# Performance work log

Measured on AMD Instinct MI355X. Metric: run time of the kernel, lower is better.

The kernel has to match this reference:

```python
import jax, jax.numpy as jnp
import numpy as np

EMBED = 1024
HIDDEN = 64  # embed_size // n_heads
B, L = 8, 4096


def setup_inputs() -> dict:
    key = jax.random.key(0)
    k1, k2, k3, k4, k5, k6, k7 = jax.random.split(key, 7)
    query = jax.random.normal(k1, (B, L, EMBED), dtype=jnp.float32)
    key_t = jax.random.normal(k2, (B, L, EMBED), dtype=jnp.float32)
    value = jax.random.normal(k3, (B, L, EMBED), dtype=jnp.float32)
    mask = jax.random.randint(k4, (B, L, L), 0, 2).astype(jnp.bool_)
    # nn.Linear(embed, hidden, bias=False) weights have shape (hidden, embed)
    s = 1.0 / np.sqrt(EMBED)
    WQ = jax.random.uniform(k5, (HIDDEN, EMBED), jnp.float32, -s, s)
    WK = jax.random.uniform(k6, (HIDDEN, EMBED), jnp.float32, -s, s)
    WV = jax.random.uniform(k7, (HIDDEN, EMBED), jnp.float32, -s, s)
    return {"query": query, "key": key_t, "value": value, "mask": mask,
            "WQ": WQ, "WK": WK, "WV": WV}


def reference(query, key, value, mask, WQ, WK, WV):
    # Projections: y = x @ W.T  (Linear without bias)
    Q = jnp.einsum('ble,he->blh', query, WQ)   # [B,L,H]
    K = jnp.einsum('ble,he->blh', key, WK)
    V = jnp.einsum('ble,he->blh', value, WV)
    scale = 1.0 / jnp.sqrt(jnp.asarray(Q.shape[-1], Q.dtype))
    scores = jnp.einsum('bqh,bkh->bqk', Q, K) * scale   # [B,L,L]
    scores = jnp.where(mask, -jnp.inf, scores)
    attn = jax.nn.softmax(scores, axis=-1)
    # dropout p=0.0 -> identity
    return jnp.einsum('bqk,bkh->bqh', attn, V)           # [B,L,H]
```

## Files before the change

### kernel.cpp

```cpp
#include <hip/hip_runtime.h>
#include <hip/hip_bf16.h>

#define NB 8
#define LL 4096
#define EE 1024
#define HH 64

typedef unsigned short u16;
typedef unsigned char u8;
typedef unsigned int u32;
typedef unsigned long long u64;
using bf16x8 = __attribute__((ext_vector_type(8))) short;
using f32x4  = __attribute__((ext_vector_type(4))) float;

__device__ __forceinline__ short f2bf(float f) {
    __hip_bfloat16 h = __float2bfloat16(f);
    return __builtin_bit_cast(short, h);
}

__device__ __forceinline__ bf16x8 pack8(const float4 a, const float4 b) {
    bf16x8 r;
    r[0] = f2bf(a.x); r[1] = f2bf(a.y); r[2] = f2bf(a.z); r[3] = f2bf(a.w);
    r[4] = f2bf(b.x); r[5] = f2bf(b.y); r[6] = f2bf(b.z); r[7] = f2bf(b.w);
    return r;
}

__global__ __launch_bounds__(256) void proj_kernel(
    const float* __restrict__ Xq, const float* __restrict__ Xk, const float* __restrict__ Xv,
    const float* __restrict__ Wq, const float* __restrict__ Wk, const float* __restrict__ Wv,
    u16* __restrict__ Oq, u16* __restrict__ Ok, u16* __restrict__ Ovt)
{
    __shared__ u16 Xs[2][64][72];
    __shared__ u16 Ws2[2][64][72];

    const int which = blockIdx.y;
    const float* X = (which == 0) ? Xq : (which == 1) ? Xk : Xv;
    const float* W = (which == 0) ? Wq : (which == 1) ? Wk : Wv;
    const float scale = (which == 0) ? 0.125f : 1.0f;

    const int tid  = threadIdx.x;
    const int lane = tid & 63;
    const int w    = tid >> 6;
    const int g    = lane >> 4;
    const int c    = lane & 15;
    const int m0   = blockIdx.x * 64;
    const int r    = tid >> 2;
    const int cb   = (tid & 3) * 16;

    const float* xrow = X + (size_t)(m0 + r) * EE + cb;
    const float* wrow = W + (size_t)r * EE + cb;

    float4 xr[4], wr[4];
    #pragma unroll
    for (int i = 0; i < 4; ++i) {
        xr[i] = reinterpret_cast<const float4*>(xrow)[i];
        wr[i] = reinterpret_cast<const float4*>(wrow)[i];
    }
    *reinterpret_cast<bf16x8*>(&Xs[0][r][cb])      = pack8(xr[0], xr[1]);
    *reinterpret_cast<bf16x8*>(&Xs[0][r][cb + 8])  = pack8(xr[2], xr[3]);
    *reinterpret_cast<bf16x8*>(&Ws2[0][r][cb])     = pack8(wr[0], wr[1]);
    *reinterpret_cast<bf16x8*>(&Ws2[0][r][cb + 8]) = pack8(wr[2], wr[3]);
    __syncthreads();

    f32x4 acc[4];
    #pragma unroll
    for (int t = 0; t < 4; ++t) acc[t] = (f32x4){0.f, 0.f, 0.f, 0.f};

    for (int s = 0; s < 16; ++s) {
        const int curb = s & 1, nxtb = curb ^ 1;
        if (s < 15) {
            #pragma unroll
            for (int i = 0; i < 4; ++i) {
                xr[i] = reinterpret_cast<const float4*>(xrow + (s + 1) * 64)[i];
                wr[i] = reinterpret_cast<const float4*>(wrow + (s + 1) * 64)[i];
            }
        }
        __builtin_amdgcn_s_setprio(1);
        #pragma unroll
        for (int kk = 0; kk < 2; ++kk) {
            bf16x8 a = *reinterpret_cast<const bf16x8*>(&Xs[curb][16*w + c][kk*32 + 8*g]);
            #pragma unroll
            for (int t = 0; t < 4; ++t) {
                bf16x8 bb = *reinterpret_cast<const bf16x8*>(&Ws2[curb][16*t + c][kk*32 + 8*g]);
                acc[t] = __builtin_amdgcn_mfma_f32_16x16x32_bf16(a, bb, acc[t], 0, 0, 0);
            }
        }
        __builtin_amdgcn_s_setprio(0);
        if (s < 15) {
            *reinterpret_cast<bf16x8*>(&Xs[nxtb][r][cb])      = pack8(xr[0], xr[1]);
            *reinterpret_cast<bf16x8*>(&Xs[nxtb][r][cb + 8])  = pack8(xr[2], xr[3]);
            *reinterpret_cast<bf16x8*>(&Ws2[nxtb][r][cb])     = pack8(wr[0], wr[1]);
            *reinterpret_cast<bf16x8*>(&Ws2[nxtb][r][cb + 8]) = pack8(wr[2], wr[3]);
        }
        __syncthreads();
    }

    if (which < 2) {
        u16* O = (which == 0) ? Oq : Ok;
        #pragma unroll
        for (int t = 0; t < 4; ++t)
            #pragma unroll
            for (int q = 0; q < 4; ++q) {
                const int mrow = m0 + 16*w + 4*g + q;
                O[(size_t)mrow * HH + 16*t + c] = (u16)f2bf(acc[t][q] * scale);
            }
    } else {
        const int bidx = m0 >> 12;
        #pragma unroll
        for (int t = 0; t < 4; ++t)
            #pragma unroll
            for (int q = 0; q < 4; ++q) {
                const int l = (m0 & (LL - 1)) + 16*w + 4*g + q;
                Ovt[((size_t)bidx * HH + 16*t + c) * LL + l] = (u16)f2bf(acc[t][q]);
            }
    }
}

__global__ __launch_bounds__(256) void attn_kernel(
    const u16* __restrict__ Qb, const u16* __restrict__ Kb, const u16* __restrict__ Vt,
    const int* __restrict__ mask, float* __restrict__ out)
{
    __shared__ u16 Ks[2][64][72];
    __shared__ u16 Vts[2][64][72];
    __shared__ u16 Ps[4][16][72];
    __shared__ u64 Pnl[2][4][64];

    const int b    = blockIdx.y;
    const int q0   = blockIdx.x * 64;
    const int tid  = threadIdx.x;
    const int lane = tid & 63;
    const int w    = tid >> 6;
    const int g    = lane >> 4;
    const int c    = lane & 15;
    const int r    = tid >> 2;
    const int cb   = (tid & 3) * 16;
    const int mrr  = tid >> 4;
    const int mcc  = tid & 15;

    const u16* kbase = Kb + (size_t)b * LL * HH;
    const u16* vbase = Vt + (size_t)b * HH * LL;
    const int* mbase0 = mask + (size_t)b * LL * LL + (size_t)(q0 + mrr) * LL + mcc * 16;

    bf16x8 qf[2];
    {
        const u16* qp = Qb + ((size_t)b * LL + q0 + 16*w + c) * HH;
        qf[0] = *reinterpret_cast<const bf16x8*>(qp + 8*g);
        qf[1] = *reinterpret_cast<const bf16x8*>(qp + 32 + 8*g);
    }

    bf16x8 kra, krb, vra, vrb;
    int4 mi0, mi1, mi2, mi3;

    #define LOADKV(kt_) do {                                                   \
        kra = *reinterpret_cast<const bf16x8*>(kbase + (size_t)((kt_)*64 + r) * HH + cb);       \
        krb = *reinterpret_cast<const bf16x8*>(kbase + (size_t)((kt_)*64 + r) * HH + cb + 8);   \
        vra = *reinterpret_cast<const bf16x8*>(vbase + (size_t)r * LL + (kt_)*64 + cb);         \
        vrb = *reinterpret_cast<const bf16x8*>(vbase + (size_t)r * LL + (kt_)*64 + cb + 8);     \
    } while (0)
    #define WRITEKV(buf_) do {                                                 \
        *reinterpret_cast<bf16x8*>(&Ks[buf_][r][cb])      = kra;               \
        *reinterpret_cast<bf16x8*>(&Ks[buf_][r][cb + 8])  = krb;               \
        *reinterpret_cast<bf16x8*>(&Vts[buf_][r][cb])     = vra;               \
        *reinterpret_cast<bf16x8*>(&Vts[buf_][r][cb + 8]) = vrb;               \
    } while (0)
    #define MLOAD(w_, p_) do {                                                 \
        const int4* _mp = reinterpret_cast<const int4*>(mbase0 + (size_t)(16*(p_)) * LL + (w_)*256); \
        mi0 = _mp[0]; mi1 = _mp[1]; mi2 = _mp[2]; mi3 = _mp[3];                \
    } while (0)
    #define MPACK(pb_, p_) do {                                                \
        u32 _bb =  (u32)(mi0.x != 0)        | ((u32)(mi0.y != 0) << 1)         \
                | ((u32)(mi0.z != 0) << 2)  | ((u32)(mi0.w != 0) << 3)         \
                | ((u32)(mi1.x != 0) << 4)  | ((u32)(mi1.y != 0) << 5)         \
                | ((u32)(mi1.z != 0) << 6)  | ((u32)(mi1.w != 0) << 7)         \
                | ((u32)(mi2.x != 0) << 8)  | ((u32)(mi2.y != 0) << 9)         \
                | ((u32)(mi2.z != 0) << 10) | ((u32)(mi2.w != 0) << 11)        \
                | ((u32)(mi3.x != 0) << 12) | ((u32)(mi3.y != 0) << 13)        \
                | ((u32)(mi3.z != 0) << 14) | ((u32)(mi3.w != 0) << 15);       \
        ((u16*)&Pnl[pb_][mcc >> 2][16*(p_) + mrr])[mcc & 3] = (u16)_bb;        \
    } while (0)

    f32x4 acc[4];
    float lpart[4];
    #pragma unroll
    for (int t = 0; t < 4; ++t) acc[t] = (f32x4){0.f, 0.f, 0.f, 0.f};
    #pragma unroll
    for (int q = 0; q < 4; ++q) lpart[q] = 0.f;

    #define TILE_BODY(CUR, PB, TI) do {                                        \
        f32x4 s[4];                                                            \
        __builtin_amdgcn_s_setprio(1);                                         \
        _Pragma("unroll")                                                      \
        for (int t = 0; t < 4; ++t) {                                          \
            s[t] = (f32x4){0.f, 0.f, 0.f, 0.f};                                \
            _Pragma("unroll")                                                  \
            for (int kk = 0; kk < 2; ++kk) {                                   \
                bf16x8 bfr = *reinterpret_cast<const bf16x8*>(&Ks[CUR][16*t + c][kk*32 + 8*g]); \
                s[t] = __builtin_amdgcn_mfma_f32_16x16x32_bf16(qf[kk], bfr, s[t], 0, 0, 0);     \
            }                                                                  \
        }                                                                      \
        __builtin_amdgcn_s_setprio(0);                                         \
        u64 mw0 = Pnl[PB][TI][16*w + 4*g + 0];                                 \
        u64 mw1 = Pnl[PB][TI][16*w + 4*g + 1];                                 \
        u64 mw2 = Pnl[PB][TI][16*w + 4*g + 2];                                 \
        u64 mw3 = Pnl[PB][TI][16*w + 4*g + 3];                                 \
        u32 mlo[4], mhi[4];                                                    \
        mlo[0] = (u32)mw0; mhi[0] = (u32)(mw0 >> 32);                          \
        mlo[1] = (u32)mw1; mhi[1] = (u32)(mw1 >> 32);                          \
        mlo[2] = (u32)mw2; mhi[2] = (u32)(mw2 >> 32);                          \
        mlo[3] = (u32)mw3; mhi[3] = (u32)(mw3 >> 32);                          \
        _Pragma("unroll")                                                      \
        for (int t = 0; t < 4; ++t)                                            \
            _Pragma("unroll")                                                  \
            for (int q = 0; q < 4; ++q) {                                      \
                u32 wsel = (t < 2) ? mlo[q] : mhi[q];                          \
                u32 bit = (wsel >> ((t & 1) * 16 + c)) & 1u;                   \
                float p = bit ? 0.f : __expf(s[t][q]);                         \
                lpart[q] += p;                                                 \
                Ps[w][4*g + q][16*t + c] = (u16)f2bf(p);                       \
            }                                                                  \
        __builtin_amdgcn_s_setprio(1);                                         \
        _Pragma("unroll")                                                      \
        for (int kk = 0; kk < 2; ++kk) {                                       \
            bf16x8 pa = *reinterpret_cast<const bf16x8*>(&Ps[w][c][kk*32 + 8*g]);               \
            _Pragma("unroll")                                                  \
            for (int t = 0; t < 4; ++t) {                                      \
                bf16x8 vfr = *reinterpret_cast<const bf16x8*>(&Vts[CUR][16*t + c][kk*32 + 8*g]);\
                acc[t] = __builtin_amdgcn_mfma_f32_16x16x32_bf16(pa, vfr, acc[t], 0, 0, 0);     \
            }                                                                  \
        }                                                                      \
        __builtin_amdgcn_s_setprio(0);                                         \
    } while (0)

    LOADKV(0);
    MLOAD(0, 0); MPACK(0, 0);
    MLOAD(0, 1); MPACK(0, 1);
    MLOAD(0, 2); MPACK(0, 2);
    MLOAD(0, 3); MPACK(0, 3);
    WRITEKV(0);
    __syncthreads();

    for (int win = 0; win < 16; ++win) {
        const int base = 4 * win;
        const int pcur = win & 1, pnxt = pcur ^ 1;
        const bool more = (win + 1 < 16);

        LOADKV(base + 1);
        if (more) MLOAD(win + 1, 0);
        TILE_BODY(0, pcur, 0);
        WRITEKV(1);
        if (more) MPACK(pnxt, 0);
        __syncthreads();

        LOADKV(base + 2);
        if (more) MLOAD(win + 1, 1);
        TILE_BODY(1, pcur, 1);
        WRITEKV(0);
        if (more) MPACK(pnxt, 1);
        __syncthreads();

        LOADKV(base + 3);
        if (more) MLOAD(win + 1, 2);
        TILE_BODY(0, pcur, 2);
        WRITEKV(1);
        if (more) MPACK(pnxt, 2);
        __syncthreads();

        if (more) { LOADKV(base + 4); MLOAD(win + 1, 3); }
        TILE_BODY(1, pcur, 3);
        if (more) { WRITEKV(0); MPACK(pnxt, 3); }
        __syncthreads();
    }

    #pragma unroll
    for (int off = 8; off >= 1; off >>= 1)
        #pragma unroll
        for (int q = 0; q < 4; ++q)
            lpart[q] += __shfl_xor(lpart[q], off, 64);
    #pragma unroll
    for (int q = 0; q < 4; ++q) {
        const float inv = 1.0f / lpart[q];
        const size_t row = (size_t)b * LL + q0 + 16*w + 4*g + q;
        #pragma unroll
        for (int t = 0; t < 4; ++t)
            out[row * HH + 16*t + c] = acc[t][q] * inv;
    }
}

extern "C" void kernel_launch(void* const* d_in, const int* in_sizes, int n_in,
                              void* d_out, int out_size, void* d_ws, size_t ws_size,
                              hipStream_t stream) {
    const float* query = (const float*)d_in[0];
    const float* key_t = (const float*)d_in[1];
    const float* value = (const float*)d_in[2];
    const int*   mask  = (const int*)d_in[3];
    const float* WQ    = (const float*)d_in[4];
    const float* WK    = (const float*)d_in[5];
    const float* WV    = (const float*)d_in[6];
    float* out = (float*)d_out;

    const size_t nqkv = (size_t)NB * LL * HH;
    u16* Qb  = (u16*)d_ws;
    u16* Kb  = Qb + nqkv;
    u16* Vtb = Kb + nqkv;

    dim3 pgrid(NB * LL / 64, 3);
    proj_kernel<<<pgrid, 256, 0, stream>>>(query, key_t, value, WQ, WK, WV, Qb, Kb, Vtb);

    dim3 agrid(LL / 64, NB);
    attn_kernel<<<agrid, 256, 0, stream>>>(Qb, Kb, Vtb, mask, out);
}
```

Measured before the change: 218.4 us.

## Process two KV tiles per barrier with swizzled unpadded LDS and per-phase mask packing

Restructures the attention main loop so each iteration prefetches and computes two 64-key tiles at a time, with four K/V LDS buffers instead of two. This halves the number of __syncthreads. LDS K/V tiles drop their padding and use an XOR swizzle to avoid bank conflicts. Mask loading changes so each thread packs 32 mask bits for its own row per phase. The cost is more registers for the doubled prefetch, which may reduce occupancy.

```diff
diff --git a/kernel.cpp b/kernel.cpp
--- a/kernel.cpp
+++ b/kernel.cpp
@@ -120,10 +120,10 @@
     const u16* __restrict__ Qb, const u16* __restrict__ Kb, const u16* __restrict__ Vt,
     const int* __restrict__ mask, float* __restrict__ out)
 {
-    __shared__ u16 Ks[2][64][72];
-    __shared__ u16 Vts[2][64][72];
+    __shared__ u16 Ks[4][64][64];
+    __shared__ u16 Vts[4][64][64];
     __shared__ u16 Ps[4][16][72];
-    __shared__ u64 Pnl[2][4][64];
+    __shared__ u64 Pnl[2][2][64];
 
     const int b    = blockIdx.y;
     const int q0   = blockIdx.x * 64;
@@ -133,13 +133,14 @@
     const int g    = lane >> 4;
     const int c    = lane & 15;
     const int r    = tid >> 2;
-    const int cb   = (tid & 3) * 16;
-    const int mrr  = tid >> 4;
-    const int mcc  = tid & 15;
+    const int ch   = tid & 3;
+    const int cb   = ch * 16;
+    const int swzw = (r & 7) << 3;
+    const int swzr = (c & 7) << 3;
 
     const u16* kbase = Kb + (size_t)b * LL * HH;
     const u16* vbase = Vt + (size_t)b * HH * LL;
-    const int* mbase0 = mask + (size_t)b * LL * LL + (size_t)(q0 + mrr) * LL + mcc * 16;
+    const int* mbase = mask + (size_t)b * LL * LL + (size_t)(q0 + r) * LL + ch * 32;
 
     bf16x8 qf[2];
     {
@@ -148,35 +149,46 @@
         qf[1] = *reinterpret_cast<const bf16x8*>(qp + 32 + 8*g);
     }
 
-    bf16x8 kra, krb, vra, vrb;
-    int4 mi0, mi1, mi2, mi3;
-
-    #define LOADKV(kt_) do {                                                   \
-        kra = *reinterpret_cast<const bf16x8*>(kbase + (size_t)((kt_)*64 + r) * HH + cb);       \
-        krb = *reinterpret_cast<const bf16x8*>(kbase + (size_t)((kt_)*64 + r) * HH + cb + 8);   \
-        vra = *reinterpret_cast<const bf16x8*>(vbase + (size_t)r * LL + (kt_)*64 + cb);         \
-        vrb = *reinterpret_cast<const bf16x8*>(vbase + (size_t)r * LL + (kt_)*64 + cb + 8);     \
-    } while (0)
-    #define WRITEKV(buf_) do {                                                 \
-        *reinterpret_cast<bf16x8*>(&Ks[buf_][r][cb])      = kra;               \
-        *reinterpret_cast<bf16x8*>(&Ks[buf_][r][cb + 8])  = krb;               \
-        *reinterpret_cast<bf16x8*>(&Vts[buf_][r][cb])     = vra;               \
-        *reinterpret_cast<bf16x8*>(&Vts[buf_][r][cb + 8]) = vrb;               \
-    } while (0)
-    #define MLOAD(w_, p_) do {                                                 \
-        const int4* _mp = reinterpret_cast<const int4*>(mbase0 + (size_t)(16*(p_)) * LL + (w_)*256); \
+    bf16x8 k0a, k0b, v0a, v0b, k1a, k1b, v1a, v1b;
+    int4 mi0, mi1, mi2, mi3, mi4, mi5, mi6, mi7;
+
+    #define LOADKV0(kt_) do {                                                  \
+        k0a = *reinterpret_cast<const bf16x8*>(kbase + (size_t)((kt_)*64 + r) * HH + cb);       \
+        k0b = *reinterpret_cast<const bf16x8*>(kbase + (size_t)((kt_)*64 + r) * HH + cb + 8);   \
+        v0a = *reinterpret_cast<const bf16x8*>(vbase + (size_t)r * LL + (kt_)*64 + cb);         \
+        v0b = *reinterpret_cast<const bf16x8*>(vbase + (size_t)r * LL + (kt_)*64 + cb + 8);     \
+    } while (0)
+    #define LOADKV1(kt_) do {                                                  \
+        k1a = *reinterpret_cast<const bf16x8*>(kbase + (size_t)((kt_)*64 + r) * HH + cb);       \
+        k1b = *reinterpret_cast<const bf16x8*>(kbase + (size_t)((kt_)*64 + r) * HH + cb + 8);   \
+        v1a = *reinterpret_cast<const bf16x8*>(vbase + (size_t)r * LL + (kt_)*64 + cb);         \
+        v1b = *reinterpret_cast<const bf16x8*>(vbase + (size_t)r * LL + (kt_)*64 + cb + 8);     \
+    } while (0)
+    #define WRITEKV0(buf_) do {                                                \
+        *reinterpret_cast<bf16x8*>(&Ks[buf_][r][cb ^ swzw])        = k0a;      \
+        *reinterpret_cast<bf16x8*>(&Ks[buf_][r][(cb ^ swzw) ^ 8])  = k0b;      \
+        *reinterpret_cast<bf16x8*>(&Vts[buf_][r][cb ^ swzw])       = v0a;      \
+        *reinterpret_cast<bf16x8*>(&Vts[buf_][r][(cb ^ swzw) ^ 8]) = v0b;      \
+    } while (0)
+    #define WRITEKV1(buf_) do {                                                \
+        *reinterpret_cast<bf16x8*>(&Ks[buf_][r][cb ^ swzw])        = k1a;      \
+        *reinterpret_cast<bf16x8*>(&Ks[buf_][r][(cb ^ swzw) ^ 8])  = k1b;      \
+        *reinterpret_cast<bf16x8*>(&Vts[buf_][r][cb ^ swzw])       = v1a;      \
+        *reinterpret_cast<bf16x8*>(&Vts[buf_][r][(cb ^ swzw) ^ 8]) = v1b;      \
+    } while (0)
+    #define MLOADPH(T_) do {                                                   \
+        const int4* _mp = reinterpret_cast<const int4*>(mbase + (T_) * 64);    \
         mi0 = _mp[0]; mi1 = _mp[1]; mi2 = _mp[2]; mi3 = _mp[3];                \
-    } while (0)
-    #define MPACK(pb_, p_) do {                                                \
-        u32 _bb =  (u32)(mi0.x != 0)        | ((u32)(mi0.y != 0) << 1)         \
-                | ((u32)(mi0.z != 0) << 2)  | ((u32)(mi0.w != 0) << 3)         \
-                | ((u32)(mi1.x != 0) << 4)  | ((u32)(mi1.y != 0) << 5)         \
-                | ((u32)(mi1.z != 0) << 6)  | ((u32)(mi1.w != 0) << 7)         \
-                | ((u32)(mi2.x != 0) << 8)  | ((u32)(mi2.y != 0) << 9)         \
-                | ((u32)(mi2.z != 0) << 10) | ((u32)(mi2.w != 0) << 11)        \
-                | ((u32)(mi3.x != 0) << 12) | ((u32)(mi3.y != 0) << 13)        \
-                | ((u32)(mi3.z != 0) << 14) | ((u32)(mi3.w != 0) << 15);       \
-        ((u16*)&Pnl[pb_][mcc >> 2][16*(p_) + mrr])[mcc & 3] = (u16)_bb;        \
+        mi4 = _mp[4]; mi5 = _mp[5]; mi6 = _mp[6]; mi7 = _mp[7];                \
+    } while (0)
+    #define PB32(v_, sh_) ( ((u32)((v_).x != 0) << (sh_))                      \
+                          | ((u32)((v_).y != 0) << ((sh_)+1))                  \
+                          | ((u32)((v_).z != 0) << ((sh_)+2))                  \
+                          | ((u32)((v_).w != 0) << ((sh_)+3)) )
+    #define MPACKPH(pb_) do {                                                  \
+        u32 _bits = PB32(mi0,0) | PB32(mi1,4)  | PB32(mi2,8)  | PB32(mi3,12)   \
+                  | PB32(mi4,16) | PB32(mi5,20) | PB32(mi6,24) | PB32(mi7,28); \
+        ((u32*)&Pnl[pb_][ch >> 1][r])[ch & 1] = _bits;                         \
     } while (0)
 
     f32x4 acc[4];
@@ -186,7 +198,7 @@
     #pragma unroll
     for (int q = 0; q < 4; ++q) lpart[q] = 0.f;
 
-    #define TILE_BODY(CUR, PB, TI) do {                                        \
+    #define TILE_BODY(BUF, PB, TI) do {                                        \
         f32x4 s[4];                                                            \
         __builtin_amdgcn_s_setprio(1);                                         \
         _Pragma("unroll")                                                      \
@@ -194,7 +206,8 @@
             s[t] = (f32x4){0.f, 0.f, 0.f, 0.f};                                \
             _Pragma("unroll")                                                  \
             for (int kk = 0; kk < 2; ++kk) {                                   \
-                bf16x8 bfr = *reinterpret_cast<const bf16x8*>(&Ks[CUR][16*t + c][kk*32 + 8*g]); \
+                bf16x8 bfr = *reinterpret_cast<const bf16x8*>(                 \
+                    &Ks[BUF][16*t + c][((kk<<5) | (g<<3)) ^ swzr]);            \
                 s[t] = __builtin_amdgcn_mfma_f32_16x16x32_bf16(qf[kk], bfr, s[t], 0, 0, 0);     \
             }                                                                  \
         }                                                                      \
@@ -221,53 +234,42 @@
         __builtin_amdgcn_s_setprio(1);                                         \
         _Pragma("unroll")                                                      \
         for (int kk = 0; kk < 2; ++kk) {                                       \
-            bf16x8 pa = *reinterpret_cast<const bf16x8*>(&Ps[w][c][kk*32 + 8*g]);               \
+            bf16x8 pfr = *reinterpret_cast<const bf16x8*>(&Ps[w][c][kk*32 + 8*g]);              \
             _Pragma("unroll")                                                  \
             for (int t = 0; t < 4; ++t) {                                      \
-                bf16x8 vfr = *reinterpret_cast<const bf16x8*>(&Vts[CUR][16*t + c][kk*32 + 8*g]);\
-                acc[t] = __builtin_amdgcn_mfma_f32_16x16x32_bf16(pa, vfr, acc[t], 0, 0, 0);     \
+                bf16x8 vfr = *reinterpret_cast<const bf16x8*>(                 \
+                    &Vts[BUF][16*t + c][((kk<<5) | (g<<3)) ^ swzr]);           \
+                acc[t] = __builtin_amdgcn_mfma_f32_16x16x32_bf16(pfr, vfr, acc[t], 0, 0, 0);    \
             }                                                                  \
         }                                                                      \
         __builtin_amdgcn_s_setprio(0);                                         \
     } while (0)
 
-    LOADKV(0);
-    MLOAD(0, 0); MPACK(0, 0);
-    MLOAD(0, 1); MPACK(0, 1);
-    MLOAD(0, 2); MPACK(0, 2);
-    MLOAD(0, 3); MPACK(0, 3);
-    WRITEKV(0);
+    LOADKV0(0);
+    LOADKV1(1);
+    MLOADPH(0);
+    WRITEKV0(0);
+    WRITEKV1(1);
+    MPACKPH(0);
     __syncthreads();
 
-    for (int win = 0; win < 16; ++win) {
-        const int base = 4 * win;
-        const int pcur = win & 1, pnxt = pcur ^ 1;
-        const bool more = (win + 1 < 16);
-
-        LOADKV(base + 1);
-        if (more) MLOAD(win + 1, 0);
-        TILE_BODY(0, pcur, 0);
-        WRITEKV(1);
-        if (more) MPACK(pnxt, 0);
-        __syncthreads();
-
-        LOADKV(base + 2);
-        if (more) MLOAD(win + 1, 1);
-        TILE_BODY(1, pcur, 1);
-        WRITEKV(0);
-        if (more) MPACK(pnxt, 1);
-        __syncthreads();
-
-        LOADKV(base + 3);
-        if (more) MLOAD(win + 1, 2);
-        TILE_BODY(0, pcur, 2);
-        WRITEKV(1);
-        if (more) MPACK(pnxt, 2);
-        __syncthreads();
-
-        if (more) { LOADKV(base + 4); MLOAD(win + 1, 3); }
-        TILE_BODY(1, pcur, 3);
-        if (more) { WRITEKV(0); MPACK(pnxt, 3); }
+    for (int f = 0; f < 32; ++f) {
+        const int pa = f & 1;
+        const int ba = (f & 1) * 2;
+        const int bn = ba ^ 2;
+
+        if (f < 31) {
+            LOADKV0(2*f + 2);
+            LOADKV1(2*f + 3);
+            MLOADPH(2*f + 2);
+        }
+        TILE_BODY(ba,     pa, 0);
+        TILE_BODY(ba + 1, pa, 1);
+        if (f < 31) {
+            WRITEKV0(bn);
+            WRITEKV1(bn + 1);
+            MPACKPH(pa ^ 1);
+        }
         __syncthreads();
     }
 
```

Result: slower. 263.7 us (+20.7%).

## Deepen mask prefetch to two stages and interleave batches in grid order

Applied to the files above, without the earlier changes.

The mask load for a tile group is now issued two tile-steps ahead using two alternating register sets (A/B), instead of one step ahead, so the global-memory latency of the large int32 mask stream has more compute to hide behind. The grid is flattened to 1D with batch index in the low bits, so neighbouring blocks work on different batches. This changes which blocks share K/V in L2 at a given time. The deeper prefetch costs an extra 16 registers per thread for the second mask buffer, which may lower occupancy.

```diff
diff --git a/kernel.cpp b/kernel.cpp
--- a/kernel.cpp
+++ b/kernel.cpp
@@ -125,8 +125,8 @@
     __shared__ u16 Ps[4][16][72];
     __shared__ u64 Pnl[2][4][64];
 
-    const int b    = blockIdx.y;
-    const int q0   = blockIdx.x * 64;
+    const int b    = blockIdx.x & 7;
+    const int q0   = (blockIdx.x >> 3) * 64;
     const int tid  = threadIdx.x;
     const int lane = tid & 63;
     const int w    = tid >> 6;
@@ -149,7 +149,7 @@
     }
 
     bf16x8 kra, krb, vra, vrb;
-    int4 mi0, mi1, mi2, mi3;
+    int4 mA0, mA1, mA2, mA3, mB0, mB1, mB2, mB3;
 
     #define LOADKV(kt_) do {                                                   \
         kra = *reinterpret_cast<const bf16x8*>(kbase + (size_t)((kt_)*64 + r) * HH + cb);       \
@@ -163,20 +163,21 @@
         *reinterpret_cast<bf16x8*>(&Vts[buf_][r][cb])     = vra;               \
         *reinterpret_cast<bf16x8*>(&Vts[buf_][r][cb + 8]) = vrb;               \
     } while (0)
-    #define MLOAD(w_, p_) do {                                                 \
-        const int4* _mp = reinterpret_cast<const int4*>(mbase0 + (size_t)(16*(p_)) * LL + (w_)*256); \
-        mi0 = _mp[0]; mi1 = _mp[1]; mi2 = _mp[2]; mi3 = _mp[3];                \
-    } while (0)
-    #define MPACK(pb_, p_) do {                                                \
-        u32 _bb =  (u32)(mi0.x != 0)        | ((u32)(mi0.y != 0) << 1)         \
-                | ((u32)(mi0.z != 0) << 2)  | ((u32)(mi0.w != 0) << 3)         \
-                | ((u32)(mi1.x != 0) << 4)  | ((u32)(mi1.y != 0) << 5)         \
-                | ((u32)(mi1.z != 0) << 6)  | ((u32)(mi1.w != 0) << 7)         \
-                | ((u32)(mi2.x != 0) << 8)  | ((u32)(mi2.y != 0) << 9)         \
-                | ((u32)(mi2.z != 0) << 10) | ((u32)(mi2.w != 0) << 11)        \
-                | ((u32)(mi3.x != 0) << 12) | ((u32)(mi3.y != 0) << 13)        \
-                | ((u32)(mi3.z != 0) << 14) | ((u32)(mi3.w != 0) << 15);       \
-        ((u16*)&Pnl[pb_][mcc >> 2][16*(p_) + mrr])[mcc & 3] = (u16)_bb;        \
+    #define MLOADX(P0, P1, P2, P3, sg) do {                                    \
+        const int4* _mp = reinterpret_cast<const int4*>(                       \
+            mbase0 + (size_t)(16 * ((sg) & 3)) * LL + ((sg) >> 2) * 256);      \
+        P0 = _mp[0]; P1 = _mp[1]; P2 = _mp[2]; P3 = _mp[3];                    \
+    } while (0)
+    #define MPACKX(P0, P1, P2, P3, sg) do {                                    \
+        u32 _bb =  (u32)(P0.x != 0)        | ((u32)(P0.y != 0) << 1)           \
+                | ((u32)(P0.z != 0) << 2)  | ((u32)(P0.w != 0) << 3)           \
+                | ((u32)(P1.x != 0) << 4)  | ((u32)(P1.y != 0) << 5)           \
+                | ((u32)(P1.z != 0) << 6)  | ((u32)(P1.w != 0) << 7)           \
+                | ((u32)(P2.x != 0) << 8)  | ((u32)(P2.y != 0) << 9)           \
+                | ((u32)(P2.z != 0) << 10) | ((u32)(P2.w != 0) << 11)          \
+                | ((u32)(P3.x != 0) << 12) | ((u32)(P3.y != 0) << 13)          \
+                | ((u32)(P3.z != 0) << 14) | ((u32)(P3.w != 0) << 15);         \
+        ((u16*)&Pnl[((sg) >> 2) & 1][mcc >> 2][16 * ((sg) & 3) + mrr])[mcc & 3] = (u16)_bb; \
     } while (0)
 
     f32x4 acc[4];
@@ -232,42 +233,30 @@
     } while (0)
 
     LOADKV(0);
-    MLOAD(0, 0); MPACK(0, 0);
-    MLOAD(0, 1); MPACK(0, 1);
-    MLOAD(0, 2); MPACK(0, 2);
-    MLOAD(0, 3); MPACK(0, 3);
+    MLOADX(mA0, mA1, mA2, mA3, 0); MPACKX(mA0, mA1, mA2, mA3, 0);
+    MLOADX(mA0, mA1, mA2, mA3, 1); MPACKX(mA0, mA1, mA2, mA3, 1);
+    MLOADX(mA0, mA1, mA2, mA3, 2); MPACKX(mA0, mA1, mA2, mA3, 2);
+    MLOADX(mA0, mA1, mA2, mA3, 3); MPACKX(mA0, mA1, mA2, mA3, 3);
+    MLOADX(mB0, mB1, mB2, mB3, 4);
     WRITEKV(0);
     __syncthreads();
 
-    for (int win = 0; win < 16; ++win) {
-        const int base = 4 * win;
-        const int pcur = win & 1, pnxt = pcur ^ 1;
-        const bool more = (win + 1 < 16);
-
-        LOADKV(base + 1);
-        if (more) MLOAD(win + 1, 0);
-        TILE_BODY(0, pcur, 0);
+    for (int it = 0; it < 32; ++it) {
+        const int f0 = 2 * it;
+        const int f1 = f0 + 1;
+
+        LOADKV(f0 + 1);
+        if (f0 <= 58) MLOADX(mA0, mA1, mA2, mA3, f0 + 5);
+        TILE_BODY(0, (f0 >> 2) & 1, f0 & 3);
         WRITEKV(1);
-        if (more) MPACK(pnxt, 0);
+        if (f0 <= 59) MPACKX(mB0, mB1, mB2, mB3, f0 + 4);
         __syncthreads();
 
-        LOADKV(base + 2);
-        if (more) MLOAD(win + 1, 1);
-        TILE_BODY(1, pcur, 1);
-        WRITEKV(0);
-        if (more) MPACK(pnxt, 1);
-        __syncthreads();
-
-        LOADKV(base + 3);
-        if (more) MLOAD(win + 1, 2);
-        TILE_BODY(0, pcur, 2);
-        WRITEKV(1);
-        if (more) MPACK(pnxt, 2);
-        __syncthreads();
-
-        if (more) { LOADKV(base + 4); MLOAD(win + 1, 3); }
-        TILE_BODY(1, pcur, 3);
-        if (more) { WRITEKV(0); MPACK(pnxt, 3); }
+        if (f1 <= 62) LOADKV(f1 + 1);
+        if (f1 <= 58) MLOADX(mB0, mB1, mB2, mB3, f1 + 5);
+        TILE_BODY(1, (f1 >> 2) & 1, f1 & 3);
+        if (f1 <= 62) WRITEKV(0);
+        if (f1 <= 59) MPACKX(mA0, mA1, mA2, mA3, f1 + 4);
         __syncthreads();
     }
 
@@ -306,6 +295,5 @@
     dim3 pgrid(NB * LL / 64, 3);
     proj_kernel<<<pgrid, 256, 0, stream>>>(query, key_t, value, WQ, WK, WV, Qb, Kb, Vtb);
 
-    dim3 agrid(LL / 64, NB);
-    attn_kernel<<<agrid, 256, 0, stream>>>(Qb, Kb, Vtb, mask, out);
-}
+    attn_kernel<<<NB * LL / 64, 256, 0, stream>>>(Qb, Kb, Vtb, mask, out);
+}
```

After: 223.9 us. 2.5% more time.
